# Kernel tuning notes

Measured on AMD Instinct MI355X. Metric: run time of the kernel, lower is better.

Reference implementation:

```python
import jax, jax.numpy as jnp
import numpy as np
import math

D_MODEL = 1024
NUM_HEADS = 16
HEAD_DIM = D_MODEL // NUM_HEADS
WINDOW = 5  # positions j with i - W//2 <= j <= i + W//2 are visible


def setup_inputs() -> dict:
    key = jax.random.key(0)
    ks = jax.random.split(key, 9)
    B, S = 2, 2048
    x = jax.random.normal(ks[0], (B, S, D_MODEL), dtype=jnp.float32)
    # Xavier-uniform linear weights [out, in] (torch convention), zero biases
    lim = math.sqrt(6.0 / (D_MODEL + D_MODEL))
    def w(k):
        return jax.random.uniform(k, (D_MODEL, D_MODEL), dtype=jnp.float32, minval=-lim, maxval=lim)
    return {
        'x': x,
        'Wq': w(ks[1]), 'bq': jnp.zeros((D_MODEL,), jnp.float32),
        'Wk': w(ks[2]), 'bk': jnp.zeros((D_MODEL,), jnp.float32),
        'Wv': w(ks[3]), 'bv': jnp.zeros((D_MODEL,), jnp.float32),
        'Wo': w(ks[4]), 'bo': jnp.zeros((D_MODEL,), jnp.float32),
    }


def reference(x, Wq, bq, Wk, bk, Wv, bv, Wo, bo):
    B, S, D = x.shape
    H, hd = NUM_HEADS, HEAD_DIM
    half = WINDOW // 2

    def proj(W, b):
        # torch Linear: y = x @ W.T + b ; split heads -> [B, H, S, hd]
        return (jnp.einsum('bsd,ed->bse', x, W) + b).reshape(B, S, H, hd).transpose(0, 2, 1, 3)

    q = proj(Wq, bq)
    k = proj(Wk, bk)
    v = proj(Wv, bv)

    scores = jnp.einsum('bhqd,bhkd->bhqk', q, k) / jnp.sqrt(jnp.asarray(hd, x.dtype))
    i = jnp.arange(S)[:, None]
    j = jnp.arange(S)[None, :]
    band = (j >= i - half) & (j <= i + half)  # [S, S] local window mask
    scores = jnp.where(band, scores, jnp.asarray(-1e9, x.dtype))
    attn = jax.nn.softmax(scores, axis=-1)  # dropout is identity in eval mode
    out = jnp.einsum('bhqk,bhkd->bhqd', attn, v)
    out = out.transpose(0, 2, 1, 3).reshape(B, S, D)
    return jnp.einsum('bsd,ed->bse', out, Wo) + bo
```

## Files before the change

### kernel.cpp

```cpp
#include <hip/hip_runtime.h>
#include <hip/hip_bf16.h>

typedef __bf16 bf16_t;
typedef __bf16 bf16x4 __attribute__((ext_vector_type(4)));
typedef __bf16 bf16x8 __attribute__((ext_vector_type(8)));
typedef float f32x4 __attribute__((ext_vector_type(4)));

#define S_LEN 2048
#define DMODEL 1024
#define NHEADS 16
#define HDIM 64
#define BROWS 4096
#define QKVN 3072

__device__ __forceinline__ void async16(const void* g, void* l) {
  __builtin_amdgcn_global_load_lds(
      (const __attribute__((address_space(1))) void*)g,
      (__attribute__((address_space(3))) void*)l, 16, 0, 0);
}

__global__ __launch_bounds__(256) void cvt_all_kernel(
    const float* __restrict__ x, const float* __restrict__ Wq,
    const float* __restrict__ Wk, const float* __restrict__ Wv,
    const float* __restrict__ Wo, bf16_t* __restrict__ dst) {
  const int i = blockIdx.x * 256 + threadIdx.x;
  constexpr int XN4 = (BROWS * DMODEL) / 4;
  constexpr int WN4 = (DMODEL * DMODEL) / 4;
  const float* src;
  size_t off;
  if (i < XN4) {
    src = x;
    off = (size_t)i;
  } else {
    const int wi = i - XN4;
    const int w = wi >> 18;
    off = (size_t)(wi & (WN4 - 1));
    src = (w == 0) ? Wq : (w == 1) ? Wk : (w == 2) ? Wv : Wo;
  }
  const float4 v = *(const float4*)(src + off * 4);
  bf16x4 o;
  o[0] = (bf16_t)v.x;
  o[1] = (bf16_t)v.y;
  o[2] = (bf16_t)v.z;
  o[3] = (bf16_t)v.w;
  *(bf16x4*)(dst + (size_t)i * 4) = o;
}

#define BARR __builtin_amdgcn_s_barrier()
#define LGKM0 asm volatile("s_waitcnt lgkmcnt(0)" ::: "memory")
#define VMC7 asm volatile("s_waitcnt vmcnt(7)" ::: "memory")
#define VMC0 asm volatile("s_waitcnt vmcnt(0)" ::: "memory")

__global__ __launch_bounds__(512, 2) void gemm_qkv256_kernel(
    const bf16_t* __restrict__ A, const bf16_t* __restrict__ W,
    const float* __restrict__ bq, const float* __restrict__ bk,
    const float* __restrict__ bv, bf16_t* __restrict__ C) {
  constexpr int Kd = 1024;
  __shared__ char lds[114688];
  char* ldsA = lds;
  char* ldsB = lds + 65536;

  const int m0 = blockIdx.x * 256;
  const int n0 = blockIdx.y * 192;

  const int tid = threadIdx.x;
  const int lane = tid & 63;
  const int wid = tid >> 6;
  const int wr = wid >> 2;
  const int wc = wid & 3;
  const int fr = lane & 15;
  const int l16 = lane >> 4;

  f32x4 acc[8][3] = {};
  bf16x8 aS0[4][2], aS1[4][2], bB[3][2];

  auto stageA = [&](int buf, int h, int kt) {
#pragma unroll
    for (int l = 0; l < 2; ++l) {
      const int idx = l * 512 + tid;
      const int r = idx >> 3;
      const int slot = idx & 7;
      async16((const char*)(A + (size_t)(m0 + h * 128 + r) * Kd + kt * 64 +
                            ((slot ^ (r & 7)) << 3)),
              ldsA + buf * 32768 + h * 16384 + r * 128 + slot * 16);
    }
  };
  auto stageB = [&](int buf, int th, int kt) {
    const int r = tid >> 3;
    const int slot = tid & 7;
    async16((const char*)(W + (size_t)(n0 + th * 64 + r) * Kd + kt * 64 +
                          ((slot ^ (r & 7)) << 3)),
            ldsB + buf * 24576 + th * 8192 + r * 128 + slot * 16);
  };

  auto rdA = [&](int buf, int row, int ks) -> bf16x8 {
    return *(const bf16x8*)(ldsA + buf * 32768 + row * 128 +
                            ((((ks << 2) + l16) ^ (row & 7)) << 4));
  };
  auto rdB = [&](int buf, int row, int ks) -> bf16x8 {
    return *(const bf16x8*)(ldsB + buf * 24576 + row * 128 +
                            ((((ks << 2) + l16) ^ (row & 7)) << 4));
  };

  stageA(0, 0, 0);
  stageA(0, 1, 0);
  stageB(0, 0, 0);
  stageB(0, 1, 0);
  stageB(0, 2, 0);
  stageA(1, 0, 1);
  stageA(1, 1, 1);
  stageB(1, 0, 1);
  stageB(1, 1, 1);
  stageB(1, 2, 1);
  VMC7;
  BARR;

#pragma unroll 1
  for (int t = 0; t < 16; ++t) {
    const int buf = t & 1;
#pragma unroll
    for (int m_ = 0; m_ < 4; ++m_)
#pragma unroll
      for (int ks_ = 0; ks_ < 2; ++ks_) {
        aS0[m_][ks_] = rdA(buf, wr * 128 + m_ * 16 + fr, ks_);
        aS1[m_][ks_] = rdA(buf, wr * 128 + 64 + m_ * 16 + fr, ks_);
      }
#pragma unroll
    for (int n_ = 0; n_ < 3; ++n_)
#pragma unroll
      for (int ks_ = 0; ks_ < 2; ++ks_)
        bB[n_][ks_] = rdB(buf, wc * 48 + n_ * 16 + fr, ks_);
    LGKM0;
    BARR;
    if (t + 2 < 16) {
      stageA(buf, 0, t + 2);
      stageA(buf, 1, t + 2);
      stageB(buf, 0, t + 2);
      stageB(buf, 1, t + 2);
      stageB(buf, 2, t + 2);
    }
    __builtin_amdgcn_s_setprio(1);
#pragma unroll
    for (int m_ = 0; m_ < 4; ++m_)
#pragma unroll
      for (int n_ = 0; n_ < 3; ++n_) {
#pragma unroll
        for (int ks_ = 0; ks_ < 2; ++ks_)
          acc[m_][n_] = __builtin_amdgcn_mfma_f32_16x16x32_bf16(
              aS0[m_][ks_], bB[n_][ks_], acc[m_][n_], 0, 0, 0);
#pragma unroll
        for (int ks_ = 0; ks_ < 2; ++ks_)
          acc[4 + m_][n_] = __builtin_amdgcn_mfma_f32_16x16x32_bf16(
              aS1[m_][ks_], bB[n_][ks_], acc[4 + m_][n_], 0, 0, 0);
      }
    __builtin_amdgcn_s_setprio(0);
    if (t < 15) {
      if (t + 2 < 16) {
        VMC7;
      } else {
        VMC0;
      }
      BARR;
    }
  }

  const int cr = l16 * 4;
#pragma unroll
  for (int nf = 0; nf < 3; ++nf) {
    const int col = n0 + wc * 48 + nf * 16 + fr;
    const int mat = col >> 10;
    const float* bp = (mat == 0) ? bq : (mat == 1) ? bk : bv;
    const float bval = bp[col & 1023];
#pragma unroll
    for (int mf = 0; mf < 8; ++mf) {
      const int row = m0 + wr * 128 + mf * 16 + cr;
#pragma unroll
      for (int r = 0; r < 4; ++r)
        C[(size_t)(row + r) * QKVN + col] = (bf16_t)(acc[mf][nf][r] + bval);
    }
  }
}

__global__ __launch_bounds__(512) void gemm_o_kernel(
    const bf16_t* __restrict__ Adat, const bf16_t* __restrict__ W,
    const float* __restrict__ bias, float* __restrict__ out) {
  constexpr int Kd = 1024, Nd = 1024, BK = 32, NT = Kd / BK;
  __shared__ bf16_t ldsA[2][128 * BK];
  __shared__ bf16_t ldsB[2][128 * BK];

  const int m0 = blockIdx.x * 128;
  const int n0 = blockIdx.y * 128;

  const int tid = threadIdx.x;
  const int lane = tid & 63;
  const int wid = tid >> 6;
  const int wr = wid >> 2;
  const int wc = wid & 3;
  const int fr = lane & 15;
  const int ko = (lane >> 4) * 8;

  f32x4 acc[4][2] = {};

  auto stage = [&](int buf, int t) {
    const int k0 = t * BK;
    const int row = tid >> 2;
    const int kb = (tid & 3) * 16;
    async16((const char*)(Adat + (size_t)(m0 + row) * Kd + k0) + kb,
            (char*)ldsA[buf] + row * 64 + kb);
    async16((const char*)(W + (size_t)(n0 + row) * Kd + k0) + kb,
            (char*)ldsB[buf] + row * 64 + kb);
  };

  auto compute = [&](int buf) {
    bf16x8 af[4], bf[2];
#pragma unroll
    for (int i = 0; i < 4; ++i)
      af[i] = *(const bf16x8*)(ldsA[buf] + (wr * 64 + i * 16 + fr) * BK + ko);
#pragma unroll
    for (int j = 0; j < 2; ++j)
      bf[j] = *(const bf16x8*)(ldsB[buf] + (wc * 32 + j * 16 + fr) * BK + ko);
#pragma unroll
    for (int i = 0; i < 4; ++i)
#pragma unroll
      for (int j = 0; j < 2; ++j)
        acc[i][j] = __builtin_amdgcn_mfma_f32_16x16x32_bf16(af[i], bf[j],
                                                            acc[i][j], 0, 0, 0);
  };

  stage(0, 0);
  __syncthreads();
#pragma unroll 1
  for (int t = 0; t < NT; ++t) {
    if (t + 1 < NT) stage((t + 1) & 1, t + 1);
    compute(t & 1);
    __syncthreads();
  }

  const int cr = (lane >> 4) * 4;
#pragma unroll
  for (int j = 0; j < 2; ++j) {
    const int col = n0 + wc * 32 + j * 16 + fr;
    const float bval = bias[col];
#pragma unroll
    for (int i = 0; i < 4; ++i) {
#pragma unroll
      for (int r = 0; r < 4; ++r) {
        const int row = m0 + wr * 64 + i * 16 + cr + r;
        out[(size_t)row * Nd + col] = acc[i][j][r] + bval;
      }
    }
  }
}

#define CHUNK 256
#define TROWS 260

__global__ __launch_bounds__(256) void attn_kernel(
    const bf16_t* __restrict__ QKV, bf16_t* __restrict__ ctx) {
  __shared__ bf16_t ldsK[TROWS * HDIM];
  __shared__ bf16_t ldsV[TROWS * HDIM];

  const int tid = threadIdx.x;
  const int blk = blockIdx.x;
  const int chunk = blk & 7;
  const int bh = blk >> 3;
  const int h = bh & (NHEADS - 1);
  const int b = bh >> 4;
  const int s0 = chunk * CHUNK;

  const bf16_t* Kb = QKV + (size_t)b * S_LEN * QKVN + DMODEL + h * HDIM;
  const bf16_t* Vb = QKV + (size_t)b * S_LEN * QKVN + 2 * DMODEL + h * HDIM;

#pragma unroll
  for (int j = 0; j < 9; ++j) {
    const int i = j * 256 + tid;
    if (i < TROWS * 8) {
      const int tr = i >> 3;
      const int slot = i & 7;
      const int c = slot ^ (tr & 7);
      int gs = s0 - 2 + tr;
      gs = (gs < 0) ? 0 : (gs >= S_LEN ? S_LEN - 1 : gs);
      async16((const char*)(Kb + (size_t)gs * QKVN) + c * 16,
              (char*)ldsK + i * 16);
      async16((const char*)(Vb + (size_t)gs * QKVN) + c * 16,
              (char*)ldsV + i * 16);
    }
  }

  const int s = s0 + tid;
  const bf16_t* Qrow = QKV + ((size_t)(b * S_LEN) + s) * QKVN + h * HDIM;
  bf16x8 q8[8];
#pragma unroll
  for (int c = 0; c < 8; ++c) q8[c] = *(const bf16x8*)(Qrow + c * 8);
  float qf[64];
#pragma unroll
  for (int c = 0; c < 8; ++c)
#pragma unroll
    for (int e = 0; e < 8; ++e) qf[c * 8 + e] = (float)q8[c][e];

  __syncthreads();

  float sc[5];
#pragma unroll
  for (int jj = 0; jj < 5; ++jj) {
    const int tr = tid + jj;
    float d = 0.f;
#pragma unroll
    for (int c = 0; c < 8; ++c) {
      const bf16x8 k8 = *(const bf16x8*)(ldsK + tr * HDIM + (c ^ (tr & 7)) * 8);
#pragma unroll
      for (int e = 0; e < 8; ++e) d += qf[c * 8 + e] * (float)k8[e];
    }
    const int j = s - 2 + jj;
    sc[jj] = (j < 0 || j >= S_LEN) ? -1e30f : d * 0.125f;
  }

  float m = sc[0];
#pragma unroll
  for (int jj = 1; jj < 5; ++jj) m = fmaxf(m, sc[jj]);
  float p[5], l = 0.f;
#pragma unroll
  for (int jj = 0; jj < 5; ++jj) {
    p[jj] = __expf(sc[jj] - m);
    l += p[jj];
  }
  const float inv = 1.0f / l;
#pragma unroll
  for (int jj = 0; jj < 5; ++jj) p[jj] *= inv;

  float o[64];
#pragma unroll
  for (int e = 0; e < 64; ++e) o[e] = 0.f;
#pragma unroll
  for (int jj = 0; jj < 5; ++jj) {
    const int tr = tid + jj;
    const float pj = p[jj];
#pragma unroll
    for (int c = 0; c < 8; ++c) {
      const bf16x8 v8 = *(const bf16x8*)(ldsV + tr * HDIM + (c ^ (tr & 7)) * 8);
#pragma unroll
      for (int e = 0; e < 8; ++e) o[c * 8 + e] += pj * (float)v8[e];
    }
  }

  bf16_t* Crow = (bf16_t*)ctx + ((size_t)(b * S_LEN) + s) * DMODEL + h * HDIM;
#pragma unroll
  for (int c = 0; c < 8; ++c) {
    bf16x8 ov;
#pragma unroll
    for (int e = 0; e < 8; ++e) ov[e] = (bf16_t)o[c * 8 + e];
    *(bf16x8*)(Crow + c * 8) = ov;
  }
}

extern "C" void kernel_launch(void* const* d_in, const int* in_sizes, int n_in,
                              void* d_out, int out_size, void* d_ws,
                              size_t ws_size, hipStream_t stream) {
  const float* x = (const float*)d_in[0];
  const float* Wq = (const float*)d_in[1];
  const float* bq = (const float*)d_in[2];
  const float* Wk = (const float*)d_in[3];
  const float* bk = (const float*)d_in[4];
  const float* Wv = (const float*)d_in[5];
  const float* bv = (const float*)d_in[6];
  const float* Wo = (const float*)d_in[7];
  const float* bo = (const float*)d_in[8];
  float* out = (float*)d_out;

  const size_t mat = (size_t)BROWS * DMODEL;
  const size_t wmat = (size_t)DMODEL * DMODEL;
  bf16_t* xb = (bf16_t*)d_ws;
  bf16_t* Wqkv = xb + mat;
  bf16_t* Wob = Wqkv + 3 * wmat;
  bf16_t* QKV = Wob + wmat;
  bf16_t* ctx = QKV + 3 * mat;

  cvt_all_kernel<<<8192, 256, 0, stream>>>(x, Wq, Wk, Wv, Wo, xb);
  gemm_qkv256_kernel<<<dim3(16, 16), 512, 0, stream>>>(xb, Wqkv, bq, bk, bv,
                                                       QKV);
  attn_kernel<<<256, 256, 0, stream>>>(QKV, ctx);
  gemm_o_kernel<<<dim3(32, 8), 512, 0, stream>>>(ctx, Wob, bo, out);
}
```

Before: 77.41 us.

## Fuse fp32-to-bf16 conversion of x into QKV GEMM A-tile staging

The separate conversion pass over x is removed. The QKV GEMM now loads fp32 x into registers, converts to bf16, and writes the swizzled tile into LDS, with the global load issued one stage ahead and the LDS write done after the MFMA block. This drops a full write and re-read of the bf16 copy of x. In exchange, each QKV block re-reads fp32 x (twice the bytes per A tile across the 16 column-blocks), holds more registers, and adds a synchronous register-to-LDS write step to the pipeline.

```diff
diff --git a/kernel.cpp b/kernel.cpp
--- a/kernel.cpp
+++ b/kernel.cpp
@@ -19,24 +19,15 @@
       (__attribute__((address_space(3))) void*)l, 16, 0, 0);
 }
 
-__global__ __launch_bounds__(256) void cvt_all_kernel(
-    const float* __restrict__ x, const float* __restrict__ Wq,
-    const float* __restrict__ Wk, const float* __restrict__ Wv,
-    const float* __restrict__ Wo, bf16_t* __restrict__ dst) {
+__global__ __launch_bounds__(256) void cvt_w_kernel(
+    const float* __restrict__ Wq, const float* __restrict__ Wk,
+    const float* __restrict__ Wv, const float* __restrict__ Wo,
+    bf16_t* __restrict__ dst) {
   const int i = blockIdx.x * 256 + threadIdx.x;
-  constexpr int XN4 = (BROWS * DMODEL) / 4;
   constexpr int WN4 = (DMODEL * DMODEL) / 4;
-  const float* src;
-  size_t off;
-  if (i < XN4) {
-    src = x;
-    off = (size_t)i;
-  } else {
-    const int wi = i - XN4;
-    const int w = wi >> 18;
-    off = (size_t)(wi & (WN4 - 1));
-    src = (w == 0) ? Wq : (w == 1) ? Wk : (w == 2) ? Wv : Wo;
-  }
+  const int w = i >> 18;
+  const size_t off = (size_t)(i & (WN4 - 1));
+  const float* src = (w == 0) ? Wq : (w == 1) ? Wk : (w == 2) ? Wv : Wo;
   const float4 v = *(const float4*)(src + off * 4);
   bf16x4 o;
   o[0] = (bf16_t)v.x;
@@ -48,11 +39,11 @@
 
 #define BARR __builtin_amdgcn_s_barrier()
 #define LGKM0 asm volatile("s_waitcnt lgkmcnt(0)" ::: "memory")
-#define VMC7 asm volatile("s_waitcnt vmcnt(7)" ::: "memory")
+#define VMC3 asm volatile("s_waitcnt vmcnt(3)" ::: "memory")
 #define VMC0 asm volatile("s_waitcnt vmcnt(0)" ::: "memory")
 
 __global__ __launch_bounds__(512, 2) void gemm_qkv256_kernel(
-    const bf16_t* __restrict__ A, const bf16_t* __restrict__ W,
+    const float* __restrict__ X, const bf16_t* __restrict__ W,
     const float* __restrict__ bq, const float* __restrict__ bk,
     const float* __restrict__ bv, bf16_t* __restrict__ C) {
   constexpr int Kd = 1024;
@@ -73,17 +64,38 @@
 
   f32x4 acc[8][3] = {};
   bf16x8 aS0[4][2], aS1[4][2], bB[3][2];
-
-  auto stageA = [&](int buf, int h, int kt) {
-#pragma unroll
-    for (int l = 0; l < 2; ++l) {
-      const int idx = l * 512 + tid;
-      const int r = idx >> 3;
-      const int slot = idx & 7;
-      async16((const char*)(A + (size_t)(m0 + h * 128 + r) * Kd + kt * 64 +
-                            ((slot ^ (r & 7)) << 3)),
-              ldsA + buf * 32768 + h * 16384 + r * 128 + slot * 16);
-    }
+  float4 aLd[8];
+
+  auto issueA = [&](int kt) {
+#pragma unroll
+    for (int h = 0; h < 2; ++h)
+#pragma unroll
+      for (int l = 0; l < 2; ++l) {
+        const int s = l * 512 + tid;
+        const int row = s >> 3, slot = s & 7;
+        const float* p =
+            X + (size_t)(m0 + h * 128 + row) * Kd + kt * 64 + slot * 8;
+        aLd[(h * 2 + l) * 2] = *(const float4*)p;
+        aLd[(h * 2 + l) * 2 + 1] = *(const float4*)(p + 4);
+      }
+  };
+  auto writeA = [&](int buf) {
+#pragma unroll
+    for (int h = 0; h < 2; ++h)
+#pragma unroll
+      for (int l = 0; l < 2; ++l) {
+        const int s = l * 512 + tid;
+        const int row = s >> 3, slot = s & 7;
+        const float4 f0 = aLd[(h * 2 + l) * 2];
+        const float4 f1 = aLd[(h * 2 + l) * 2 + 1];
+        bf16x8 v;
+        v[0] = (bf16_t)f0.x; v[1] = (bf16_t)f0.y;
+        v[2] = (bf16_t)f0.z; v[3] = (bf16_t)f0.w;
+        v[4] = (bf16_t)f1.x; v[5] = (bf16_t)f1.y;
+        v[6] = (bf16_t)f1.z; v[7] = (bf16_t)f1.w;
+        *(bf16x8*)(ldsA + buf * 32768 + h * 16384 + row * 128 +
+                   ((slot ^ (row & 7)) << 4)) = v;
+      }
   };
   auto stageB = [&](int buf, int th, int kt) {
     const int r = tid >> 3;
@@ -102,18 +114,19 @@
                             ((((ks << 2) + l16) ^ (row & 7)) << 4));
   };
 
-  stageA(0, 0, 0);
-  stageA(0, 1, 0);
+  issueA(0);
   stageB(0, 0, 0);
   stageB(0, 1, 0);
   stageB(0, 2, 0);
-  stageA(1, 0, 1);
-  stageA(1, 1, 1);
   stageB(1, 0, 1);
   stageB(1, 1, 1);
   stageB(1, 2, 1);
-  VMC7;
+  writeA(0);
+  issueA(1);
+  VMC0;
+  LGKM0;
   BARR;
+  writeA(1);
 
 #pragma unroll 1
   for (int t = 0; t < 16; ++t) {
@@ -130,11 +143,10 @@
 #pragma unroll
       for (int ks_ = 0; ks_ < 2; ++ks_)
         bB[n_][ks_] = rdB(buf, wc * 48 + n_ * 16 + fr, ks_);
+    if (t + 2 < 16) issueA(t + 2);
     LGKM0;
     BARR;
     if (t + 2 < 16) {
-      stageA(buf, 0, t + 2);
-      stageA(buf, 1, t + 2);
       stageB(buf, 0, t + 2);
       stageB(buf, 1, t + 2);
       stageB(buf, 2, t + 2);
@@ -156,10 +168,12 @@
     __builtin_amdgcn_s_setprio(0);
     if (t < 15) {
       if (t + 2 < 16) {
-        VMC7;
+        VMC3;
       } else {
         VMC0;
       }
+      if (t + 2 < 16) writeA(buf);
+      LGKM0;
       BARR;
     }
   }
@@ -369,14 +383,13 @@
 
   const size_t mat = (size_t)BROWS * DMODEL;
   const size_t wmat = (size_t)DMODEL * DMODEL;
-  bf16_t* xb = (bf16_t*)d_ws;
-  bf16_t* Wqkv = xb + mat;
+  bf16_t* Wqkv = (bf16_t*)d_ws;
   bf16_t* Wob = Wqkv + 3 * wmat;
   bf16_t* QKV = Wob + wmat;
   bf16_t* ctx = QKV + 3 * mat;
 
-  cvt_all_kernel<<<8192, 256, 0, stream>>>(x, Wq, Wk, Wv, Wo, xb);
-  gemm_qkv256_kernel<<<dim3(16, 16), 512, 0, stream>>>(xb, Wqkv, bq, bk, bv,
+  cvt_w_kernel<<<4096, 256, 0, stream>>>(Wq, Wk, Wv, Wo, Wqkv);
+  gemm_qkv256_kernel<<<dim3(16, 16), 512, 0, stream>>>(x, Wqkv, bq, bk, bv,
                                                        QKV);
   attn_kernel<<<256, 256, 0, stream>>>(QKV, ctx);
   gemm_o_kernel<<<dim3(32, 8), 512, 0, stream>>>(ctx, Wob, bo, out);
```

New measurement: 79.35 us. 2.5% more time.

## Shrink QKV GEMM tile to 128x192 with 4 waves per block

Applied to the files above, without the earlier changes.

The QKV projection GEMM moves from 256x192 tiles with 8 waves to 128x192 tiles with 4 waves, each wave computing 64x96. The grid doubles to 512 blocks, so there are more blocks than the 256 CUs, which should improve CU coverage and wave balance. LDS use drops so more blocks can be resident per CU. The cost is less A/B reuse per block, higher global-to-LDS traffic, and more fragment loads per MFMA. The wait counts are adjusted to match the new number of async loads.

```diff
diff --git a/kernel.cpp b/kernel.cpp
--- a/kernel.cpp
+++ b/kernel.cpp
@@ -48,53 +48,57 @@
 
 #define BARR __builtin_amdgcn_s_barrier()
 #define LGKM0 asm volatile("s_waitcnt lgkmcnt(0)" ::: "memory")
-#define VMC7 asm volatile("s_waitcnt vmcnt(7)" ::: "memory")
+#define VMC10 asm volatile("s_waitcnt vmcnt(10)" ::: "memory")
 #define VMC0 asm volatile("s_waitcnt vmcnt(0)" ::: "memory")
 
-__global__ __launch_bounds__(512, 2) void gemm_qkv256_kernel(
+__global__ __launch_bounds__(256, 2) void gemm_qkv_kernel(
     const bf16_t* __restrict__ A, const bf16_t* __restrict__ W,
     const float* __restrict__ bq, const float* __restrict__ bk,
     const float* __restrict__ bv, bf16_t* __restrict__ C) {
   constexpr int Kd = 1024;
-  __shared__ char lds[114688];
+  __shared__ char lds[81920];
   char* ldsA = lds;
-  char* ldsB = lds + 65536;
-
-  const int m0 = blockIdx.x * 256;
+  char* ldsB = lds + 32768;
+
+  const int m0 = blockIdx.x * 128;
   const int n0 = blockIdx.y * 192;
 
   const int tid = threadIdx.x;
   const int lane = tid & 63;
   const int wid = tid >> 6;
-  const int wr = wid >> 2;
-  const int wc = wid & 3;
+  const int wr = wid >> 1;
+  const int wc = wid & 1;
   const int fr = lane & 15;
   const int l16 = lane >> 4;
 
-  f32x4 acc[8][3] = {};
-  bf16x8 aS0[4][2], aS1[4][2], bB[3][2];
-
-  auto stageA = [&](int buf, int h, int kt) {
-#pragma unroll
-    for (int l = 0; l < 2; ++l) {
-      const int idx = l * 512 + tid;
+  f32x4 acc[4][6] = {};
+  bf16x8 aS[4][2], bB[6][2];
+
+  auto stageA = [&](int buf, int kt) {
+#pragma unroll
+    for (int l = 0; l < 4; ++l) {
+      const int idx = l * 256 + tid;
       const int r = idx >> 3;
       const int slot = idx & 7;
-      async16((const char*)(A + (size_t)(m0 + h * 128 + r) * Kd + kt * 64 +
+      async16((const char*)(A + (size_t)(m0 + r) * Kd + kt * 64 +
                             ((slot ^ (r & 7)) << 3)),
-              ldsA + buf * 32768 + h * 16384 + r * 128 + slot * 16);
-    }
-  };
-  auto stageB = [&](int buf, int th, int kt) {
-    const int r = tid >> 3;
-    const int slot = tid & 7;
-    async16((const char*)(W + (size_t)(n0 + th * 64 + r) * Kd + kt * 64 +
-                          ((slot ^ (r & 7)) << 3)),
-            ldsB + buf * 24576 + th * 8192 + r * 128 + slot * 16);
+              ldsA + buf * 16384 + r * 128 + slot * 16);
+    }
+  };
+  auto stageB = [&](int buf, int kt) {
+#pragma unroll
+    for (int l = 0; l < 6; ++l) {
+      const int idx = l * 256 + tid;
+      const int r = idx >> 3;
+      const int slot = idx & 7;
+      async16((const char*)(W + (size_t)(n0 + r) * Kd + kt * 64 +
+                            ((slot ^ (r & 7)) << 3)),
+              ldsB + buf * 24576 + r * 128 + slot * 16);
+    }
   };
 
   auto rdA = [&](int buf, int row, int ks) -> bf16x8 {
-    return *(const bf16x8*)(ldsA + buf * 32768 + row * 128 +
+    return *(const bf16x8*)(ldsA + buf * 16384 + row * 128 +
                             ((((ks << 2) + l16) ^ (row & 7)) << 4));
   };
   auto rdB = [&](int buf, int row, int ks) -> bf16x8 {
@@ -102,17 +106,11 @@
                             ((((ks << 2) + l16) ^ (row & 7)) << 4));
   };
 
-  stageA(0, 0, 0);
-  stageA(0, 1, 0);
-  stageB(0, 0, 0);
-  stageB(0, 1, 0);
-  stageB(0, 2, 0);
-  stageA(1, 0, 1);
-  stageA(1, 1, 1);
-  stageB(1, 0, 1);
-  stageB(1, 1, 1);
-  stageB(1, 2, 1);
-  VMC7;
+  stageA(0, 0);
+  stageB(0, 0);
+  stageA(1, 1);
+  stageB(1, 1);
+  VMC10;
   BARR;
 
 #pragma unroll 1
@@ -121,42 +119,32 @@
 #pragma unroll
     for (int m_ = 0; m_ < 4; ++m_)
 #pragma unroll
-      for (int ks_ = 0; ks_ < 2; ++ks_) {
-        aS0[m_][ks_] = rdA(buf, wr * 128 + m_ * 16 + fr, ks_);
-        aS1[m_][ks_] = rdA(buf, wr * 128 + 64 + m_ * 16 + fr, ks_);
-      }
-#pragma unroll
-    for (int n_ = 0; n_ < 3; ++n_)
-#pragma unroll
       for (int ks_ = 0; ks_ < 2; ++ks_)
-        bB[n_][ks_] = rdB(buf, wc * 48 + n_ * 16 + fr, ks_);
+        aS[m_][ks_] = rdA(buf, wr * 64 + m_ * 16 + fr, ks_);
+#pragma unroll
+    for (int n_ = 0; n_ < 6; ++n_)
+#pragma unroll
+      for (int ks_ = 0; ks_ < 2; ++ks_)
+        bB[n_][ks_] = rdB(buf, wc * 96 + n_ * 16 + fr, ks_);
     LGKM0;
     BARR;
     if (t + 2 < 16) {
-      stageA(buf, 0, t + 2);
-      stageA(buf, 1, t + 2);
-      stageB(buf, 0, t + 2);
-      stageB(buf, 1, t + 2);
-      stageB(buf, 2, t + 2);
+      stageA(buf, t + 2);
+      stageB(buf, t + 2);
     }
     __builtin_amdgcn_s_setprio(1);
 #pragma unroll
     for (int m_ = 0; m_ < 4; ++m_)
 #pragma unroll
-      for (int n_ = 0; n_ < 3; ++n_) {
+      for (int n_ = 0; n_ < 6; ++n_)
 #pragma unroll
         for (int ks_ = 0; ks_ < 2; ++ks_)
           acc[m_][n_] = __builtin_amdgcn_mfma_f32_16x16x32_bf16(
-              aS0[m_][ks_], bB[n_][ks_], acc[m_][n_], 0, 0, 0);
-#pragma unroll
-        for (int ks_ = 0; ks_ < 2; ++ks_)
-          acc[4 + m_][n_] = __builtin_amdgcn_mfma_f32_16x16x32_bf16(
-              aS1[m_][ks_], bB[n_][ks_], acc[4 + m_][n_], 0, 0, 0);
-      }
+              aS[m_][ks_], bB[n_][ks_], acc[m_][n_], 0, 0, 0);
     __builtin_amdgcn_s_setprio(0);
     if (t < 15) {
       if (t + 2 < 16) {
-        VMC7;
+        VMC10;
       } else {
         VMC0;
       }
@@ -166,14 +154,14 @@
 
   const int cr = l16 * 4;
 #pragma unroll
-  for (int nf = 0; nf < 3; ++nf) {
-    const int col = n0 + wc * 48 + nf * 16 + fr;
+  for (int nf = 0; nf < 6; ++nf) {
+    const int col = n0 + wc * 96 + nf * 16 + fr;
     const int mat = col >> 10;
     const float* bp = (mat == 0) ? bq : (mat == 1) ? bk : bv;
     const float bval = bp[col & 1023];
 #pragma unroll
-    for (int mf = 0; mf < 8; ++mf) {
-      const int row = m0 + wr * 128 + mf * 16 + cr;
+    for (int mf = 0; mf < 4; ++mf) {
+      const int row = m0 + wr * 64 + mf * 16 + cr;
 #pragma unroll
       for (int r = 0; r < 4; ++r)
         C[(size_t)(row + r) * QKVN + col] = (bf16_t)(acc[mf][nf][r] + bval);
@@ -376,8 +364,8 @@
   bf16_t* ctx = QKV + 3 * mat;
 
   cvt_all_kernel<<<8192, 256, 0, stream>>>(x, Wq, Wk, Wv, Wo, xb);
-  gemm_qkv256_kernel<<<dim3(16, 16), 512, 0, stream>>>(xb, Wqkv, bq, bk, bv,
-                                                       QKV);
+  gemm_qkv_kernel<<<dim3(32, 16), 256, 0, stream>>>(xb, Wqkv, bq, bk, bv,
+                                                    QKV);
   attn_kernel<<<256, 256, 0, stream>>>(QKV, ctx);
   gemm_o_kernel<<<dim3(32, 8), 512, 0, stream>>>(ctx, Wob, bo, out);
 }
```

Measured after the change: 73.39 us. 5.2% less time.
